# Optimization experiments

Hardware: AMD Instinct MI355X
Metric: run time of the kernel (lower is better)

The kernel has to match this reference:

```python
import jax, jax.numpy as jnp
import numpy as np

T, H, I, E, TOP_K = 4096, 2048, 1024, 16, 2
I_SHARED = 1024  # moe_intermediate_size * n_shared_experts


def _silu_and_mul(gu):
    g, u = jnp.split(gu, 2, axis=-1)
    return jax.nn.silu(g) * u


def setup_inputs() -> dict:
    key = jax.random.key(0)
    ks = jax.random.split(key, 8)
    s = 0.02
    return {
        "hidden_states": jax.random.normal(ks[0], (T, H), jnp.float32),
        "gate_w": jax.random.normal(ks[1], (E, H), jnp.float32) * s,          # router
        "w1": jax.random.normal(ks[2], (E, 2 * I, H), jnp.float32) * s,       # expert gate_up
        "b1": jax.random.normal(ks[3], (E, 2 * I), jnp.float32) * s,
        "w2": jax.random.normal(ks[4], (E, H, I), jnp.float32) * s,           # expert down
        "sg_w": jax.random.normal(ks[5], (2 * I_SHARED, H), jnp.float32) * s, # shared gate_up
        "sg_b": jax.random.normal(ks[6], (2 * I_SHARED,), jnp.float32) * s,
        "sd_w": jax.random.normal(ks[7], (H, I_SHARED), jnp.float32) * s,     # shared down
    }


def reference(hidden_states, gate_w, w1, b1, w2, sg_w, sg_b, sd_w):
    x = hidden_states  # [T, H]

    # shared expert MLP (gate_up has bias, down does not)
    shared = _silu_and_mul(x @ sg_w.T + sg_b) @ sd_w.T  # [T, H]

    # router: softmax -> top-k -> renormalize (norm_topk_prob=True)
    probs = jax.nn.softmax(x @ gate_w.T, axis=-1)       # [T, E]
    wts, idx = jax.lax.top_k(probs, TOP_K)              # [T, k]
    wts = wts / jnp.sum(wts, axis=-1, keepdims=True)

    # per-expert combine coefficient: coef[e, t] = sum_k wts[t,k] * (idx[t,k]==e)
    coef = jnp.sum(jax.nn.one_hot(idx, E, dtype=x.dtype) * wts[..., None], axis=1).T  # [E, T]

    def body(acc, params):
        w1e, b1e, w2e, ce = params
        a = _silu_and_mul(x @ w1e.T + b1e)   # [T, I]
        return acc + ce[:, None] * (a @ w2e.T), None

    out, _ = jax.lax.scan(body, jnp.zeros_like(x), (w1, b1, w2, coef))
    return out + shared
```

## Files before the change

kernel.cpp:

```cpp
#include <hip/hip_runtime.h>
#include <hip/hip_bf16.h>
#include <stdint.h>

#define T_TOK 4096
#define H_DIM 2048
#define I_DIM 1024
#define NEXP  16
#define NROWS 16384

typedef short bf16x8 __attribute__((ext_vector_type(8)));
typedef float f32x4  __attribute__((ext_vector_type(4)));
typedef unsigned short u16;

__device__ __forceinline__ u16 f2b(float f) {
  union { __hip_bfloat16 h; u16 u; } cv;
  cv.h = __float2bfloat16(f);
  return cv.u;
}

__device__ __forceinline__ void gload16(const void* g, void* l) {
  __builtin_amdgcn_global_load_lds((const __attribute__((address_space(1))) void*)g,
                                   (__attribute__((address_space(3))) void*)l, 16, 0, 0);
}

__device__ __forceinline__ bf16x8 cvt_frag2(const float* pLo, const float* pHi) {
  f32x4 v0 = *(const f32x4*)pLo;
  f32x4 v1 = *(const f32x4*)pHi;
  bf16x8 o;
  o[0] = (short)f2b(v0[0]); o[1] = (short)f2b(v0[1]);
  o[2] = (short)f2b(v0[2]); o[3] = (short)f2b(v0[3]);
  o[4] = (short)f2b(v1[0]); o[5] = (short)f2b(v1[1]);
  o[6] = (short)f2b(v1[2]); o[7] = (short)f2b(v1[3]);
  return o;
}

__global__ __launch_bounds__(256) void router_kernel(const float* __restrict__ x,
                                                     const float* __restrict__ gw,
                                                     int* __restrict__ sel,
                                                     float* __restrict__ selw,
                                                     int* __restrict__ counts,
                                                     u16* __restrict__ x_bf) {
  int t = blockIdx.x;
  int tid = threadIdx.x;
  const float* xr = x + (size_t)t * H_DIM;
  double p[NEXP];
#pragma unroll
  for (int e = 0; e < NEXP; ++e) p[e] = 0.0;
  bf16x8 xs;
#pragma unroll
  for (int j = 0; j < 8; ++j) {
    int h = tid * 8 + j;
    float xf = xr[h];
    xs[j] = (short)f2b(xf);
    double xv = (double)xf;
#pragma unroll
    for (int e = 0; e < NEXP; ++e) p[e] += xv * (double)gw[e * H_DIM + h];
  }
  *(bf16x8*)(x_bf + (size_t)t * H_DIM + tid * 8) = xs;
#pragma unroll
  for (int e = 0; e < NEXP; ++e) {
#pragma unroll
    for (int off = 32; off > 0; off >>= 1) p[e] += __shfl_down(p[e], off);
  }
  __shared__ double sm[4][NEXP];
  int w = tid >> 6;
  if ((tid & 63) == 0) {
#pragma unroll
    for (int e = 0; e < NEXP; ++e) sm[w][e] = p[e];
  }
  __syncthreads();
  if (tid == 0) {
    double l0 = -1e300, l1 = -1e300;
    int e0 = 0, e1 = 0;
    for (int e = 0; e < NEXP; ++e) {
      double v = sm[0][e] + sm[1][e] + sm[2][e] + sm[3][e];
      if (v > l0) { l1 = l0; e1 = e0; l0 = v; e0 = e; }
      else if (v > l1) { l1 = v; e1 = e; }
    }
    double w0 = 1.0 / (1.0 + exp(l1 - l0));
    sel[t * 2 + 0] = e0;
    sel[t * 2 + 1] = e1;
    selw[t * 2 + 0] = (float)w0;
    selw[t * 2 + 1] = (float)(1.0 - w0);
    atomicAdd(&counts[e0], 1);
    atomicAdd(&counts[e1], 1);
  }
}

__global__ void prefix_kernel(const int* __restrict__ counts, int* __restrict__ rowbase) {
  if (threadIdx.x == 0 && blockIdx.x == 0) {
    int acc = 0;
    for (int e = 0; e < NEXP; ++e) {
      rowbase[e] = acc;
      acc += (counts[e] + 127) & ~127;
    }
    rowbase[NEXP] = acc;
  }
}

__global__ __launch_bounds__(256) void scatter_kernel(const int* __restrict__ sel,
                                                      const float* __restrict__ selw,
                                                      const int* __restrict__ rowbase,
                                                      int* __restrict__ cursor,
                                                      int* __restrict__ tok_of_row,
                                                      float* __restrict__ coef_of_row,
                                                      int* __restrict__ row_of_tok) {
  int idx = blockIdx.x * 256 + threadIdx.x;
  if (idx < T_TOK * 2) {
    int t = idx >> 1;
    int e = sel[idx];
    int slot = atomicAdd(&cursor[e], 1);
    int row = rowbase[e] + slot;
    tok_of_row[row] = t;
    coef_of_row[row] = selw[idx];
    row_of_tok[idx] = row;
  } else if (idx < T_TOK * 3) {
    int t = idx - T_TOK * 2;
    int sb = rowbase[NEXP];
    tok_of_row[sb + t] = t;
    coef_of_row[sb + t] = 1.0f;
  }
}


__global__ __launch_bounds__(256, 3) void gemm1_kernel(
    const u16* __restrict__ x_bf, const float* __restrict__ w1,
    const float* __restrict__ sg_w,
    const float* __restrict__ b1, const float* __restrict__ sg_b,
    const int* __restrict__ tok_of_row, const int* __restrict__ counts,
    const int* __restrict__ rowbase, u16* __restrict__ abuf) {
  int nt = blockIdx.x, rt = blockIdx.y, e = blockIdx.z;
  int n_e = (e < NEXP) ? counts[e] : T_TOK;
  if (rt * 128 >= n_e) return;
  int rbase = rowbase[e];
  int n_valid = n_e - rt * 128;
  if (n_valid > 128) n_valid = 128;

  __shared__ short As[128 * 64];
  __shared__ float Bsf[128 * 64];
  __shared__ int Ts[128];

  int tid = threadIdx.x;
  if (tid < 128)
    Ts[tid] = (rt * 128 + tid < n_e) ? tok_of_row[rbase + rt * 128 + tid] : 0;
  __syncthreads();

  int wavebase = tid & 0xC0;
  const u16* srcA[4];
  short* dstA[4];
#pragma unroll
  for (int p = 0; p < 4; ++p) {
    int c = p * 256 + tid;
    int r = c >> 3;
    int koff = ((c & 7) * 8) ^ ((r & 7) << 3);
    int tok = Ts[r];
    srcA[p] = x_bf + (size_t)tok * H_DIM + koff;
    dstA[p] = &As[(p * 256 + wavebase) * 8];
  }
  const float* Wexp = (e < NEXP) ? (w1 + (size_t)e * (2 * I_DIM) * H_DIM) : sg_w;
  const float* srcB[8];
  float* dstB[8];
#pragma unroll
  for (int p = 0; p < 8; ++p) {
    int c = p * 256 + tid;
    int r = c >> 4;
    int eoff = ((c & 15) ^ (r & 15)) * 4;
    int gr = (r < 64) ? (nt * 64 + r) : (I_DIM + nt * 64 + (r - 64));
    srcB[p] = Wexp + (size_t)gr * H_DIM + eoff;
    dstB[p] = &Bsf[(p * 256 + wavebase) * 4];
  }

  f32x4 acc[4][4];
#pragma unroll
  for (int m = 0; m < 4; ++m)
#pragma unroll
    for (int n = 0; n < 4; ++n) acc[m][n] = (f32x4){0.f, 0.f, 0.f, 0.f};

  int lane = tid & 63, w = tid >> 6, wr = w >> 1, wc = w & 1;
  int laneq = lane & 15, hi = lane >> 4;

  for (int kt = 0; kt < H_DIM / 64; ++kt) {
    if (kt) __syncthreads();
#pragma unroll
    for (int p = 0; p < 4; ++p) gload16(srcA[p] + kt * 64, dstA[p]);
#pragma unroll
    for (int p = 0; p < 8; ++p) gload16(srcB[p] + kt * 64, dstB[p]);
    __syncthreads();
#pragma unroll
    for (int ks = 0; ks < 2; ++ks) {
      bf16x8 a[4], b[4];
#pragma unroll
      for (int f = 0; f < 4; ++f) {
        int rowA = wr * 64 + f * 16 + laneq;
        a[f] = *(const bf16x8*)(As + rowA * 64 + ((ks * 32 + hi * 8) ^ ((rowA & 7) << 3)));
        int rowB = ((f < 2) ? (wc * 32 + f * 16) : (64 + wc * 32 + (f - 2) * 16)) + laneq;
        int s0 = (ks * 8 + hi * 2) ^ (rowB & 15);
        const float* pB = Bsf + rowB * 64;
        b[f] = cvt_frag2(pB + s0 * 4, pB + (s0 ^ 1) * 4);
      }
#pragma unroll
      for (int f = 0; f < 4; ++f)
#pragma unroll
        for (int fn = 0; fn < 4; ++fn)
          acc[f][fn] = __builtin_amdgcn_mfma_f32_16x16x32_bf16(a[f], b[fn], acc[f][fn], 0, 0, 0);
    }
  }

  const float* bias = (e < NEXP) ? (b1 + (size_t)e * (2 * I_DIM)) : sg_b;
#pragma unroll
  for (int nf = 0; nf < 2; ++nf) {
    int j = nt * 64 + wc * 32 + nf * 16 + laneq;
    float bg = bias[j];
    float bu = bias[I_DIM + j];
#pragma unroll
    for (int mf = 0; mf < 4; ++mf) {
#pragma unroll
      for (int reg = 0; reg < 4; ++reg) {
        int r = wr * 64 + mf * 16 + hi * 4 + reg;
        if (r < n_valid) {
          float g = acc[mf][nf][reg] + bg;
          float u = acc[mf][nf + 2][reg] + bu;
          float s = g / (1.0f + __expf(-g));
          abuf[(size_t)(rbase + rt * 128 + r) * I_DIM + j] = f2b(s * u);
        }
      }
    }
  }
}

__global__ __launch_bounds__(256, 3) void gemm2_kernel(
    const u16* __restrict__ abuf, const float* __restrict__ w2,
    const float* __restrict__ sd_w,
    const int* __restrict__ tok_of_row, const float* __restrict__ coef_of_row,
    const int* __restrict__ counts, const int* __restrict__ rowbase,
    float* __restrict__ y, float* __restrict__ out) {
  int nt = blockIdx.x, rt = blockIdx.y, e = blockIdx.z;
  int n_e = (e < NEXP) ? counts[e] : T_TOK;
  if (rt * 128 >= n_e) return;
  int rbase = rowbase[e];
  int n_valid = n_e - rt * 128;
  if (n_valid > 128) n_valid = 128;

  __shared__ short As[128 * 64];
  __shared__ float Bsf[128 * 64];
  __shared__ int Ts[128];
  __shared__ float Cs[128];

  int tid = threadIdx.x;
  if (tid < 128) {
    bool valid = rt * 128 + tid < n_e;
    int row = rbase + rt * 128 + tid;
    Ts[tid] = valid ? tok_of_row[row] : 0;
    Cs[tid] = valid ? coef_of_row[row] : 0.0f;
  }
  __syncthreads();

  int wavebase = tid & 0xC0;
  const u16* srcA[4];
  short* dstA[4];
#pragma unroll
  for (int p = 0; p < 4; ++p) {
    int c = p * 256 + tid;
    int r = c >> 3;
    int koff = ((c & 7) * 8) ^ ((r & 7) << 3);
    srcA[p] = abuf + (size_t)(rbase + rt * 128 + r) * I_DIM + koff;
    dstA[p] = &As[(p * 256 + wavebase) * 8];
  }
  const float* Wexp = (e < NEXP) ? (w2 + (size_t)e * H_DIM * I_DIM) : sd_w;
  const float* srcB[8];
  float* dstB[8];
#pragma unroll
  for (int p = 0; p < 8; ++p) {
    int c = p * 256 + tid;
    int r = c >> 4;
    int eoff = ((c & 15) ^ (r & 15)) * 4;
    srcB[p] = Wexp + (size_t)(nt * 128 + r) * I_DIM + eoff;
    dstB[p] = &Bsf[(p * 256 + wavebase) * 4];
  }

  f32x4 acc[4][4];
#pragma unroll
  for (int m = 0; m < 4; ++m)
#pragma unroll
    for (int n = 0; n < 4; ++n) acc[m][n] = (f32x4){0.f, 0.f, 0.f, 0.f};

  int lane = tid & 63, w = tid >> 6, wr = w >> 1, wc = w & 1;
  int laneq = lane & 15, hi = lane >> 4;

  for (int kt = 0; kt < I_DIM / 64; ++kt) {
    if (kt) __syncthreads();
#pragma unroll
    for (int p = 0; p < 4; ++p) gload16(srcA[p] + kt * 64, dstA[p]);
#pragma unroll
    for (int p = 0; p < 8; ++p) gload16(srcB[p] + kt * 64, dstB[p]);
    __syncthreads();
#pragma unroll
    for (int ks = 0; ks < 2; ++ks) {
      bf16x8 a[4], b[4];
#pragma unroll
      for (int f = 0; f < 4; ++f) {
        int rowA = wr * 64 + f * 16 + laneq;
        int rowB = wc * 64 + f * 16 + laneq;
        a[f] = *(const bf16x8*)(As + rowA * 64 + ((ks * 32 + hi * 8) ^ ((rowA & 7) << 3)));
        int s0 = (ks * 8 + hi * 2) ^ (rowB & 15);
        const float* pB = Bsf + rowB * 64;
        b[f] = cvt_frag2(pB + s0 * 4, pB + (s0 ^ 1) * 4);
      }
#pragma unroll
      for (int f = 0; f < 4; ++f)
#pragma unroll
        for (int fn = 0; fn < 4; ++fn)
          acc[f][fn] = __builtin_amdgcn_mfma_f32_16x16x32_bf16(a[f], b[fn], acc[f][fn], 0, 0, 0);
    }
  }

#pragma unroll
  for (int mf = 0; mf < 4; ++mf) {
#pragma unroll
    for (int nf = 0; nf < 4; ++nf) {
      int col = nt * 128 + wc * 64 + nf * 16 + laneq;
#pragma unroll
      for (int reg = 0; reg < 4; ++reg) {
        int r = wr * 64 + mf * 16 + hi * 4 + reg;
        if (r < n_valid) {
          float val = acc[mf][nf][reg] * Cs[r];
          if (e < NEXP)
            y[(size_t)(rbase + rt * 128 + r) * H_DIM + col] = val;
          else
            out[(size_t)Ts[r] * H_DIM + col] = val;
        }
      }
    }
  }
}

__global__ __launch_bounds__(256) void combine_kernel(float* __restrict__ out,
                                                      const float* __restrict__ y,
                                                      const int* __restrict__ row_of_tok) {
  int t = blockIdx.x;
  int r0 = row_of_tok[t * 2];
  int r1 = row_of_tok[t * 2 + 1];
  const float* y0 = y + (size_t)r0 * H_DIM;
  const float* y1 = y + (size_t)r1 * H_DIM;
  float* o = out + (size_t)t * H_DIM;
  int c = threadIdx.x * 8;
#pragma unroll
  for (int h = 0; h < 2; ++h) {
    float4 ov = *(float4*)(o + c + h * 4);
    float4 a = *(const float4*)(y0 + c + h * 4);
    float4 b = *(const float4*)(y1 + c + h * 4);
    ov.x += a.x + b.x; ov.y += a.y + b.y; ov.z += a.z + b.z; ov.w += a.w + b.w;
    *(float4*)(o + c + h * 4) = ov;
  }
}

extern "C" void kernel_launch(void* const* d_in, const int* in_sizes, int n_in,
                              void* d_out, int out_size, void* d_ws, size_t ws_size,
                              hipStream_t stream) {
  const float* x    = (const float*)d_in[0];
  const float* gate_w = (const float*)d_in[1];
  const float* w1   = (const float*)d_in[2];
  const float* b1   = (const float*)d_in[3];
  const float* w2   = (const float*)d_in[4];
  const float* sg_w = (const float*)d_in[5];
  const float* sg_b = (const float*)d_in[6];
  const float* sd_w = (const float*)d_in[7];
  float* out = (float*)d_out;

  uint8_t* ws = (uint8_t*)d_ws;
  size_t off = 0;
  auto alloc = [&](size_t bytes) -> void* {
    void* p = ws + off;
    off += (bytes + 255) & ~(size_t)255;
    return p;
  };
  u16*  x_bf  = (u16*)alloc((size_t)T_TOK * H_DIM * 2);
  u16*  abuf  = (u16*)alloc((size_t)NROWS * I_DIM * 2);
  float* y    = (float*)alloc((size_t)NROWS * H_DIM * 4);
  int*  tok_of_row  = (int*)alloc((size_t)NROWS * 4);
  float* coef_of_row = (float*)alloc((size_t)NROWS * 4);
  int*  row_of_tok  = (int*)alloc((size_t)T_TOK * 2 * 4);
  int*  sel   = (int*)alloc((size_t)T_TOK * 2 * 4);
  float* selw = (float*)alloc((size_t)T_TOK * 2 * 4);
  int*  counts  = (int*)alloc(256);
  int*  cursor  = (int*)alloc(256);
  int*  rowbase = (int*)alloc(256);
  (void)ws_size; (void)in_sizes; (void)n_in; (void)out_size;

  hipMemsetAsync(counts, 0, 512, stream);

  router_kernel<<<dim3(T_TOK), dim3(256), 0, stream>>>(x, gate_w, sel, selw, counts, x_bf);
  prefix_kernel<<<dim3(1), dim3(64), 0, stream>>>(counts, rowbase);
  scatter_kernel<<<dim3(48), dim3(256), 0, stream>>>(sel, selw, rowbase, cursor,
                                                     tok_of_row, coef_of_row, row_of_tok);

  gemm1_kernel<<<dim3(16, 32, 17), dim3(256), 0, stream>>>(
      x_bf, w1, sg_w, b1, sg_b, tok_of_row, counts, rowbase, abuf);

  gemm2_kernel<<<dim3(16, 32, 17), dim3(256), 0, stream>>>(
      abuf, w2, sd_w, tok_of_row, coef_of_row, counts, rowbase, y, out);

  combine_kernel<<<dim3(T_TOK), dim3(256), 0, stream>>>(out, y, row_of_tok);
}
```

Measured before the change: 458.2 us.

## Pre-convert down-proj weights to bf16 inside gemm1 and load bf16 in gemm2

Extra z-slice blocks in gemm1 convert all expert and shared down-projection weights (w2, sd_w) from fp32 to a bf16 buffer, running alongside the gate_up GEMM. gemm2 then streams bf16 weights straight into LDS with the same swizzle as the activations. This halves B-tile LDS footprint and removes the per-fragment fp32→bf16 conversion, which lets gemm2 raise its occupancy hint to 4. The cost is an extra full read of w2 in fp32 plus a bf16 write and re-read every call, and 512 conversion blocks competing with gemm1 tiles.

Result: no change. 453.5 us (-1.0%).

```diff
diff --git a/kernel.cpp b/kernel.cpp
--- a/kernel.cpp
+++ b/kernel.cpp
@@ -11,6 +11,7 @@
 typedef short bf16x8 __attribute__((ext_vector_type(8)));
 typedef float f32x4  __attribute__((ext_vector_type(4)));
 typedef unsigned short u16;
+typedef unsigned short u16x8 __attribute__((ext_vector_type(8)));
 
 __device__ __forceinline__ u16 f2b(float f) {
   union { __hip_bfloat16 h; u16 u; } cv;
@@ -25,7 +26,7 @@
 
 __device__ __forceinline__ bf16x8 cvt_frag2(const float* pLo, const float* pHi) {
   f32x4 v0 = *(const f32x4*)pLo;
-  f32x4 v1 = *(const f32x4*)pHi;
+  f32x4 v1 = *(const f32x4*)(pHi);
   bf16x8 o;
   o[0] = (short)f2b(v0[0]); o[1] = (short)f2b(v0[1]);
   o[2] = (short)f2b(v0[2]); o[3] = (short)f2b(v0[3]);
@@ -122,14 +123,37 @@
   }
 }
 
-
 __global__ __launch_bounds__(256, 3) void gemm1_kernel(
     const u16* __restrict__ x_bf, const float* __restrict__ w1,
     const float* __restrict__ sg_w,
     const float* __restrict__ b1, const float* __restrict__ sg_b,
     const int* __restrict__ tok_of_row, const int* __restrict__ counts,
-    const int* __restrict__ rowbase, u16* __restrict__ abuf) {
-  int nt = blockIdx.x, rt = blockIdx.y, e = blockIdx.z;
+    const int* __restrict__ rowbase, u16* __restrict__ abuf,
+    const float* __restrict__ w2, const float* __restrict__ sd_w,
+    u16* __restrict__ W2cat) {
+  int tid = threadIdx.x;
+
+  if (blockIdx.z == 0) {
+    const int N2 = 16 * 2048 * 1024 / 8;
+    const int N3 = 2048 * 1024 / 8;
+    int lin = blockIdx.y * 16 + blockIdx.x;
+    int gid = lin * 256 + tid;
+    int stride = 512 * 256;
+    u16x8* dst = (u16x8*)W2cat;
+    for (int i = gid; i < N2 + N3; i += stride) {
+      const float4* s = (i < N2) ? ((const float4*)w2 + 2 * (size_t)i)
+                                 : ((const float4*)sd_w + 2 * (size_t)(i - N2));
+      float4 v0 = s[0];
+      float4 v1 = s[1];
+      u16x8 o;
+      o[0] = f2b(v0.x); o[1] = f2b(v0.y); o[2] = f2b(v0.z); o[3] = f2b(v0.w);
+      o[4] = f2b(v1.x); o[5] = f2b(v1.y); o[6] = f2b(v1.z); o[7] = f2b(v1.w);
+      dst[i] = o;
+    }
+    return;
+  }
+
+  int nt = blockIdx.x, rt = blockIdx.y, e = blockIdx.z - 1;
   int n_e = (e < NEXP) ? counts[e] : T_TOK;
   if (rt * 128 >= n_e) return;
   int rbase = rowbase[e];
@@ -140,7 +164,6 @@
   __shared__ float Bsf[128 * 64];
   __shared__ int Ts[128];
 
-  int tid = threadIdx.x;
   if (tid < 128)
     Ts[tid] = (rt * 128 + tid < n_e) ? tok_of_row[rbase + rt * 128 + tid] : 0;
   __syncthreads();
@@ -228,9 +251,8 @@
   }
 }
 
-__global__ __launch_bounds__(256, 3) void gemm2_kernel(
-    const u16* __restrict__ abuf, const float* __restrict__ w2,
-    const float* __restrict__ sd_w,
+__global__ __launch_bounds__(256, 4) void gemm2_kernel(
+    const u16* __restrict__ abuf, const u16* __restrict__ W2cat,
     const int* __restrict__ tok_of_row, const float* __restrict__ coef_of_row,
     const int* __restrict__ counts, const int* __restrict__ rowbase,
     float* __restrict__ y, float* __restrict__ out) {
@@ -242,7 +264,7 @@
   if (n_valid > 128) n_valid = 128;
 
   __shared__ short As[128 * 64];
-  __shared__ float Bsf[128 * 64];
+  __shared__ short Bs[128 * 64];
   __shared__ int Ts[128];
   __shared__ float Cs[128];
 
@@ -256,8 +278,13 @@
   __syncthreads();
 
   int wavebase = tid & 0xC0;
+  const u16* Wb = W2cat + ((e < NEXP)
+      ? ((size_t)e * H_DIM + nt * 128) * I_DIM
+      : ((size_t)NEXP * H_DIM * I_DIM + (size_t)(nt * 128) * I_DIM));
   const u16* srcA[4];
   short* dstA[4];
+  const u16* srcB[4];
+  short* dstB[4];
 #pragma unroll
   for (int p = 0; p < 4; ++p) {
     int c = p * 256 + tid;
@@ -265,17 +292,8 @@
     int koff = ((c & 7) * 8) ^ ((r & 7) << 3);
     srcA[p] = abuf + (size_t)(rbase + rt * 128 + r) * I_DIM + koff;
     dstA[p] = &As[(p * 256 + wavebase) * 8];
-  }
-  const float* Wexp = (e < NEXP) ? (w2 + (size_t)e * H_DIM * I_DIM) : sd_w;
-  const float* srcB[8];
-  float* dstB[8];
-#pragma unroll
-  for (int p = 0; p < 8; ++p) {
-    int c = p * 256 + tid;
-    int r = c >> 4;
-    int eoff = ((c & 15) ^ (r & 15)) * 4;
-    srcB[p] = Wexp + (size_t)(nt * 128 + r) * I_DIM + eoff;
-    dstB[p] = &Bsf[(p * 256 + wavebase) * 4];
+    srcB[p] = Wb + (size_t)r * I_DIM + koff;
+    dstB[p] = &Bs[(p * 256 + wavebase) * 8];
   }
 
   f32x4 acc[4][4];
@@ -292,7 +310,7 @@
 #pragma unroll
     for (int p = 0; p < 4; ++p) gload16(srcA[p] + kt * 64, dstA[p]);
 #pragma unroll
-    for (int p = 0; p < 8; ++p) gload16(srcB[p] + kt * 64, dstB[p]);
+    for (int p = 0; p < 4; ++p) gload16(srcB[p] + kt * 64, dstB[p]);
     __syncthreads();
 #pragma unroll
     for (int ks = 0; ks < 2; ++ks) {
@@ -302,9 +320,7 @@
         int rowA = wr * 64 + f * 16 + laneq;
         int rowB = wc * 64 + f * 16 + laneq;
         a[f] = *(const bf16x8*)(As + rowA * 64 + ((ks * 32 + hi * 8) ^ ((rowA & 7) << 3)));
-        int s0 = (ks * 8 + hi * 2) ^ (rowB & 15);
-        const float* pB = Bsf + rowB * 64;
-        b[f] = cvt_frag2(pB + s0 * 4, pB + (s0 ^ 1) * 4);
+        b[f] = *(const bf16x8*)(Bs + rowB * 64 + ((ks * 32 + hi * 8) ^ ((rowB & 7) << 3)));
       }
 #pragma unroll
       for (int f = 0; f < 4; ++f)
@@ -374,6 +390,7 @@
     off += (bytes + 255) & ~(size_t)255;
     return p;
   };
+  u16*  W2cat = (u16*)alloc((size_t)17 * 2048 * 1024 * 2);
   u16*  x_bf  = (u16*)alloc((size_t)T_TOK * H_DIM * 2);
   u16*  abuf  = (u16*)alloc((size_t)NROWS * I_DIM * 2);
   float* y    = (float*)alloc((size_t)NROWS * H_DIM * 4);
@@ -394,11 +411,11 @@
   scatter_kernel<<<dim3(48), dim3(256), 0, stream>>>(sel, selw, rowbase, cursor,
                                                      tok_of_row, coef_of_row, row_of_tok);
 
-  gemm1_kernel<<<dim3(16, 32, 17), dim3(256), 0, stream>>>(
-      x_bf, w1, sg_w, b1, sg_b, tok_of_row, counts, rowbase, abuf);
+  gemm1_kernel<<<dim3(16, 32, 18), dim3(256), 0, stream>>>(
+      x_bf, w1, sg_w, b1, sg_b, tok_of_row, counts, rowbase, abuf, w2, sd_w, W2cat);
 
   gemm2_kernel<<<dim3(16, 32, 17), dim3(256), 0, stream>>>(
-      abuf, w2, sd_w, tok_of_row, coef_of_row, counts, rowbase, y, out);
+      abuf, W2cat, tok_of_row, coef_of_row, counts, rowbase, y, out);
 
   combine_kernel<<<dim3(T_TOK), dim3(256), 0, stream>>>(out, y, row_of_tok);
 }
```
